# Performance work log

Measured on AMD Instinct MI355X. Metric: run time of the kernel, lower is better.

Reference implementation:

```python
import jax, jax.numpy as jnp
import numpy as np


def setup_inputs() -> dict:
    key = jax.random.key(0)
    ks = jax.random.split(key, 6)
    B, T, I, H, O = 64, 512, 256, 512, 256
    stdv = 1.0 / np.sqrt(H)
    u = lambda k, shape: jax.random.uniform(k, shape, jnp.float32, -stdv, stdv)
    return {
        "x": jax.random.normal(ks[0], (B, T, I), jnp.float32),
        "W": u(ks[1], (I, 4 * H)),
        "U": u(ks[2], (H, 4 * H)),
        "bias": u(ks[3], (4 * H,)),
        "Wl": u(ks[4], (H, O)),
        "bl": u(ks[5], (O,)),
    }


def lstm_scan(x, W, U, bias):
    B, T, I = x.shape
    H = U.shape[0]
    # Precompute input projections for all timesteps in one big GEMM: [B,T,4H]
    x_proj = jnp.einsum("bti,ig->btg", x, W) + bias

    def step(carry, xp_t):
        h, c = carry
        gates = xp_t + h @ U  # [B, 4H]
        i_t = jax.nn.sigmoid(gates[:, :H])
        f_t = jax.nn.sigmoid(gates[:, H:2 * H])
        g_t = jnp.tanh(gates[:, 2 * H:3 * H])
        o_t = jax.nn.sigmoid(gates[:, 3 * H:])
        c_new = f_t * c + i_t * g_t
        h_new = o_t * jnp.tanh(c_new)
        return (h_new, c_new), h_new

    h0 = jnp.zeros((B, H), x.dtype)
    c0 = jnp.zeros((B, H), x.dtype)
    (h_T, c_T), hs = jax.lax.scan(step, (h0, c0), jnp.swapaxes(x_proj, 0, 1))
    hidden_seq = jnp.swapaxes(hs, 0, 1)  # [B, T, H]
    return hidden_seq, h_T, c_T


def reference(x, W, U, bias, Wl, bl):
    hidden_seq, h_T, c_T = lstm_scan(x, W, U, bias)
    out = hidden_seq @ Wl + bl  # [B, T, O]
    return out, (h_T, c_T)
```

## Files before the change

### kernel.cpp

```cpp
#include <hip/hip_runtime.h>
#include <stdint.h>

typedef uint16_t u16;
typedef uint32_t u32;
typedef unsigned long long u64;
typedef __attribute__((ext_vector_type(8))) __bf16 bf16x8;
typedef __attribute__((ext_vector_type(8))) short short8;
typedef __attribute__((ext_vector_type(4))) float floatx4;

__device__ __forceinline__ float bf2f(u16 u) {
  union { u32 i; float f; } v; v.i = ((u32)u) << 16; return v.f;
}
__device__ __forceinline__ u16 f2bf(float f) {
  union { float f; u32 i; } v; v.f = f;
  u32 i = v.i;
  return (u16)((i + 0x7FFFu + ((i >> 16) & 1u)) >> 16);
}
__device__ __forceinline__ float sigm(float x) { return 1.f / (1.f + __expf(-x)); }
__device__ __forceinline__ float tanh_f(float x) {
  x = fminf(15.f, fmaxf(-15.f, x));
  float e = __expf(2.f * x);
  return (e - 1.f) / (e + 1.f);
}

__global__ void transpose_f32_bf16(const float* __restrict__ src, u16* __restrict__ dst,
                                   int R, int C) {
  __shared__ u16 tile[32][33];
  int x = blockIdx.x * 32 + threadIdx.x;
#pragma unroll
  for (int j = 0; j < 4; ++j) {
    int y = blockIdx.y * 32 + threadIdx.y + j * 8;
    if (x < C && y < R) tile[threadIdx.y + j * 8][threadIdx.x] = f2bf(src[(size_t)y * C + x]);
  }
  __syncthreads();
  int x2 = blockIdx.y * 32 + threadIdx.x;
#pragma unroll
  for (int j = 0; j < 4; ++j) {
    int y2 = blockIdx.x * 32 + threadIdx.y + j * 8;
    if (x2 < R && y2 < C) dst[(size_t)y2 * R + x2] = tile[threadIdx.x][threadIdx.y + j * 8];
  }
}

#define T_STEPS 512
#define HLSZ (16 * 520)
#define NWORK 224

#define LSTM_STEP(XC, XN, TT)                                                  \
  {                                                                            \
    const int t = (TT);                                                        \
    const int tn = (t + 1) & (T_STEPS - 1);                                    \
          \
    if (((tn) & 63) == 0 && t < T_STEPS - 1) {                                 \
      _Pragma("unroll")                                                        \
      for (int r = 0; r < 4; ++r) {                                            \
        const u32* cc = ctr + ((g * 16 + q4 * 4 + r) * 8 + (tn >> 6));         \
        while (__hip_atomic_load(cc, __ATOMIC_RELAXED,                         \
                                 __HIP_MEMORY_SCOPE_AGENT) < 32u)              \
          __builtin_amdgcn_s_sleep(2);                                         \
      }                                                                        \
      __asm__ volatile("" ::: "memory");                                       \
    }                                                                          \
                   \
    _Pragma("unroll")                                                          \
    for (int qg = 0; qg < 4; ++qg)                                             \
      _Pragma("unroll")                                                        \
      for (int r = 0; r < 4; ++r)                                              \
        XN[qg * 4 + r] = xp_base[((size_t)(q4 * 4 + r) * T_STEPS + tn) * 2048  \
                                 + qg * 512 + cb + n];                         \
    __asm__ volatile("" ::: "memory");                                         \
    floatx4 acc[4] = {};                                                       \
    if (t > 0) {                                                               \
      const u64* hsrc = (const u64*)(hT_all)                                   \
                        + (size_t)(g * T_STEPS + (t - 1)) * 2048;              \
      u64 v[8];                                                                \
      for (;;) {                                                               \
        _Pragma("unroll")                                                      \
        for (int it = 0; it < 8; ++it)                                         \
          v[it] = __hip_atomic_load(hsrc + it * 256 + tid, __ATOMIC_RELAXED,   \
                                    __HIP_MEMORY_SCOPE_AGENT);                 \
        bool ok = true;                                                        \
        _Pragma("unroll")                                                      \
        for (int it = 0; it < 8; ++it) ok &= (v[it] != ~0ull);                 \
        if (ok) break;                                                         \
      }                                                                        \
      __asm__ volatile("" ::: "memory");                                       \
      u16* buf = hls + ((t - 1) & 1) * HLSZ;                                   \
      _Pragma("unroll")                                                        \
      for (int it = 0; it < 8; ++it) {                                         \
        int idx = it * 256 + tid;                                              \
        int tile = idx >> 6, w = idx & 63;                                     \
        *(u64*)(buf + (w >> 2) * 520 + tile * 16 + (w & 3) * 4) = v[it];       \
      }                                                                        \
      __syncthreads();                                                         \
      _Pragma("unroll")                                                        \
      for (int kt = 0; kt < 16; ++kt) {                                        \
        bf16x8 a = *(const bf16x8*)(buf + n * 520 + kt * 32 + q4 * 8);         \
        acc[0] = __builtin_amdgcn_mfma_f32_16x16x32_bf16(a, u[0][kt], acc[0], 0, 0, 0); \
        acc[1] = __builtin_amdgcn_mfma_f32_16x16x32_bf16(a, u[1][kt], acc[1], 0, 0, 0); \
        acc[2] = __builtin_amdgcn_mfma_f32_16x16x32_bf16(a, u[2][kt], acc[2], 0, 0, 0); \
        acc[3] = __builtin_amdgcn_mfma_f32_16x16x32_bf16(a, u[3][kt], acc[3], 0, 0, 0); \
      }                                                                        \
    }                                                                          \
    _Pragma("unroll")                                                          \
    for (int r = 0; r < 4; ++r) {                                              \
      float gi = sigm(acc[0][r] + bf2f(XC[r]));                                \
      float gf = sigm(acc[1][r] + bf2f(XC[4 + r]));                            \
      float gg = tanh_f(acc[2][r] + bf2f(XC[8 + r]));                          \
      float go = sigm(acc[3][r] + bf2f(XC[12 + r]));                           \
      float cn = gf * cst[r] + gi * gg;                                        \
      cst[r] = cn;                                                             \
      float hv = go * tanh_f(cn);                                              \
      int row = q4 * 4 + r;                                                    \
      hp[row * 16 + n] = f2bf(hv);                                             \
      if (t == T_STEPS - 1) {                                                  \
        out_hT[(g * 16 + row) * 512 + cb + n] = hv;                            \
        out_cT[(g * 16 + row) * 512 + cb + n] = cn;                            \
      }                                                                        \
    }                                                                          \
    __asm__ volatile("s_waitcnt lgkmcnt(0)" ::: "memory");                     \
    {                                                                          \
      u64 v = *(const u64*)(hp + (lane >> 2) * 16 + (lane & 3) * 4);           \
      u64* hdst = (u64*)(hT_all) + (size_t)(g * T_STEPS + t) * 2048            \
                  + p * 64 + lane;                                             \
      __hip_atomic_store(hdst, v, __ATOMIC_RELAXED, __HIP_MEMORY_SCOPE_AGENT); \
    }                                                                          \
  }

__global__ __launch_bounds__(256, 1) void fused_lstm(
    const float* __restrict__ x,
    const u16* __restrict__ WT,
    const float* __restrict__ bias,
    u16* __restrict__ xp,
    const u16* __restrict__ UT,
    u16* __restrict__ hT_all,
    const u16* __restrict__ WlT,
    const float* __restrict__ bl,
    float* __restrict__ outC,
    float* __restrict__ out_hT,
    float* __restrict__ out_cT,
    u32* __restrict__ ctr) {
  __shared__ __align__(16) u16 smem[2 * HLSZ + 4 * 256];
  const int bi = blockIdx.x;
  const int tid = threadIdx.x;

  if (bi >= 32) {
    u16* As = smem;
    u16* Bs = smem + 64 * 40;
    const int wid = bi - 32;
    const int wave = tid >> 6, lane = tid & 63;
    const int q4 = lane >> 4, n16 = lane & 15;
    const int mw = (wave >> 1) * 32, nw = (wave & 1) * 32;
    const int ldrow = tid >> 2, ldseg = (tid & 3) * 8;

    for (int j = wid; j < 16384; j += NWORK) {
      const int tch = j >> 11;
      const int rem = j & 2047;
      const int b = rem >> 5, nt = rem & 31;
      const int m0 = b * 512 + tch * 64, n0 = nt * 64;
      floatx4 acc[2][2] = {};
      for (int k0 = 0; k0 < 256; k0 += 32) {
        const float* ap = x + (size_t)(m0 + ldrow) * 256 + k0 + ldseg;
        floatx4 a0 = *(const floatx4*)ap;
        floatx4 a1 = *(const floatx4*)(ap + 4);
        short8 s;
        s[0] = (short)f2bf(a0[0]); s[1] = (short)f2bf(a0[1]);
        s[2] = (short)f2bf(a0[2]); s[3] = (short)f2bf(a0[3]);
        s[4] = (short)f2bf(a1[0]); s[5] = (short)f2bf(a1[1]);
        s[6] = (short)f2bf(a1[2]); s[7] = (short)f2bf(a1[3]);
        *(short8*)(As + ldrow * 40 + ldseg) = s;
        *(short8*)(Bs + ldrow * 40 + ldseg) =
            *(const short8*)(WT + (size_t)(n0 + ldrow) * 256 + k0 + ldseg);
        __syncthreads();
#pragma unroll
        for (int mi = 0; mi < 2; ++mi) {
          bf16x8 a = *(const bf16x8*)(As + (mw + mi * 16 + n16) * 40 + q4 * 8);
#pragma unroll
          for (int ni = 0; ni < 2; ++ni) {
            bf16x8 bb = *(const bf16x8*)(Bs + (nw + ni * 16 + n16) * 40 + q4 * 8);
            acc[mi][ni] = __builtin_amdgcn_mfma_f32_16x16x32_bf16(a, bb, acc[mi][ni], 0, 0, 0);
          }
        }
        __syncthreads();
      }
#pragma unroll
      for (int mi = 0; mi < 2; ++mi)
#pragma unroll
        for (int ni = 0; ni < 2; ++ni) {
          int col = n0 + nw + ni * 16 + n16;
          float bv = bias[col];
#pragma unroll
          for (int r = 0; r < 4; ++r) {
            int m = m0 + mw + mi * 16 + q4 * 4 + r;
            u16 val = f2bf(acc[mi][ni][r] + bv);
            __hip_atomic_store(xp + (size_t)m * 2048 + col, val,
                               __ATOMIC_RELAXED, __HIP_MEMORY_SCOPE_AGENT);
          }
        }
      __asm__ volatile("s_waitcnt vmcnt(0)" ::: "memory");
      __syncthreads();
      if (tid == 0)
        __hip_atomic_fetch_add(ctr + b * 8 + tch, 1u,
                               __ATOMIC_RELAXED, __HIP_MEMORY_SCOPE_AGENT);
    }

    for (int j = wid; j < 2048; j += NWORK) {
      const int tb = j >> 4, g2 = (j >> 2) & 3, nt = j & 3;
      const int m0 = g2 * 8192 + tb * 64, n0 = nt * 64;
      const int mm = m0 + ldrow;
      const size_t slot = ((size_t)((mm >> 13) * 512 + ((mm & 8191) >> 4))) * 8192
                          + (mm & 15) * 16;
      floatx4 acc[2][2] = {};
      for (int k0 = 0; k0 < 512; k0 += 32) {
        int kk = k0 + ldseg;
        const u64* ap64 = (const u64*)(hT_all + slot + (kk >> 4) * 256 + (kk & 15));
        u64 lo, hi;
        for (;;) {
          lo = __hip_atomic_load(ap64, __ATOMIC_RELAXED, __HIP_MEMORY_SCOPE_AGENT);
          hi = __hip_atomic_load(ap64 + 1, __ATOMIC_RELAXED, __HIP_MEMORY_SCOPE_AGENT);
          if (lo != ~0ull && hi != ~0ull) break;
          __builtin_amdgcn_s_sleep(8);
        }
        *(u64*)(As + ldrow * 40 + ldseg) = lo;
        *(u64*)(As + ldrow * 40 + ldseg + 4) = hi;
        *(short8*)(Bs + ldrow * 40 + ldseg) =
            *(const short8*)(WlT + (size_t)(n0 + ldrow) * 512 + k0 + ldseg);
        __syncthreads();
#pragma unroll
        for (int mi = 0; mi < 2; ++mi) {
          bf16x8 a = *(const bf16x8*)(As + (mw + mi * 16 + n16) * 40 + q4 * 8);
#pragma unroll
          for (int ni = 0; ni < 2; ++ni) {
            bf16x8 bb = *(const bf16x8*)(Bs + (nw + ni * 16 + n16) * 40 + q4 * 8);
            acc[mi][ni] = __builtin_amdgcn_mfma_f32_16x16x32_bf16(a, bb, acc[mi][ni], 0, 0, 0);
          }
        }
        __syncthreads();
      }
#pragma unroll
      for (int mi = 0; mi < 2; ++mi)
#pragma unroll
        for (int ni = 0; ni < 2; ++ni) {
          int col = n0 + nw + ni * 16 + n16;
          float bv = bl[col];
#pragma unroll
          for (int r = 0; r < 4; ++r) {
            int m = m0 + mw + mi * 16 + q4 * 4 + r;
            int orow = ((m >> 13) * 16 + (m & 15)) * 512 + ((m & 8191) >> 4);
            outC[(size_t)orow * 256 + col] = acc[mi][ni][r] + bv;
          }
        }
    }
    return;
  }

  u16* hls = smem;
  u16* hstw = smem + 2 * HLSZ;
  const int g = (bi & 7) >> 1;
  const int wgi = ((bi & 1) << 2) | (bi >> 3);
  const int wave = tid >> 6;
  const int lane = tid & 63;
  const int n = lane & 15;
  const int q4 = lane >> 4;
  const int cb = wgi * 64 + wave * 16;
  const int p = wgi * 4 + wave;
  u16* hp = hstw + wave * 256;

  bf16x8 u[4][16];
#pragma unroll
  for (int qg = 0; qg < 4; ++qg) {
    const u16* up = UT + (size_t)(qg * 512 + cb + n) * 512;
#pragma unroll
    for (int kt = 0; kt < 16; ++kt)
      u[qg][kt] = *(const bf16x8*)(up + kt * 32 + q4 * 8);
  }

  float cst[4] = {0.f, 0.f, 0.f, 0.f};
  const u16* xp_base = xp + (size_t)(g * 16) * T_STEPS * 2048;

#pragma unroll
  for (int r = 0; r < 4; ++r) {
    const u32* cc = ctr + ((g * 16 + q4 * 4 + r) * 8 + 0);
    while (__hip_atomic_load(cc, __ATOMIC_RELAXED, __HIP_MEMORY_SCOPE_AGENT) < 32u)
      __builtin_amdgcn_s_sleep(2);
  }
  __asm__ volatile("" ::: "memory");

  u16 xa[16], xb[16];
#pragma unroll
  for (int qg = 0; qg < 4; ++qg)
#pragma unroll
    for (int r = 0; r < 4; ++r)
      xa[qg * 4 + r] = xp_base[((size_t)(q4 * 4 + r) * T_STEPS + 0) * 2048
                               + qg * 512 + cb + n];

#pragma unroll 1
  for (int t2 = 0; t2 < T_STEPS; t2 += 2) {
    LSTM_STEP(xa, xb, t2)
    LSTM_STEP(xb, xa, t2 + 1)
  }
}

extern "C" void kernel_launch(void* const* d_in, const int* in_sizes, int n_in,
                              void* d_out, int out_size, void* d_ws, size_t ws_size,
                              hipStream_t stream) {
  (void)in_sizes; (void)n_in; (void)out_size; (void)ws_size;
  const float* x    = (const float*)d_in[0];
  const float* W    = (const float*)d_in[1];
  const float* U    = (const float*)d_in[2];
  const float* bias = (const float*)d_in[3];
  const float* Wl   = (const float*)d_in[4];
  const float* bl   = (const float*)d_in[5];
  float* out = (float*)d_out;
  char* ws = (char*)d_ws;

  u16* xp     = (u16*)(ws + 0);
  u16* UT     = (u16*)(ws + 134217728);
  u16* WT     = (u16*)(ws + 136314880);
  u16* WlT    = (u16*)(ws + 137363456);
  u16* hT_all = (u16*)(ws + 137625600);

  u32* ctr = (u32*)(out + 8388608);

  hipMemsetAsync(hT_all, 0xFF, 33554432, stream);
  hipMemsetAsync(ctr, 0x00, 2048, stream);

  transpose_f32_bf16<<<dim3(2048 / 32, 256 / 32), dim3(32, 8), 0, stream>>>(W, WT, 256, 2048);
  transpose_f32_bf16<<<dim3(2048 / 32, 512 / 32), dim3(32, 8), 0, stream>>>(U, UT, 512, 2048);
  transpose_f32_bf16<<<dim3(256 / 32, 512 / 32), dim3(32, 8), 0, stream>>>(Wl, WlT, 512, 256);

  fused_lstm<<<256, 256, 0, stream>>>(x, WT, bias, xp, UT, hT_all, WlT, bl,
                                      out, out + 8388608, out + 8421376, ctr);
}
```

Measured before the change: 1.441 ms.

## Fuse weight transposes into persistent kernel and add per-step progress counters

```diff
diff --git a/kernel.cpp b/kernel.cpp
--- a/kernel.cpp
+++ b/kernel.cpp
@@ -23,24 +23,6 @@
   return (e - 1.f) / (e + 1.f);
 }
 
-__global__ void transpose_f32_bf16(const float* __restrict__ src, u16* __restrict__ dst,
-                                   int R, int C) {
-  __shared__ u16 tile[32][33];
-  int x = blockIdx.x * 32 + threadIdx.x;
-#pragma unroll
-  for (int j = 0; j < 4; ++j) {
-    int y = blockIdx.y * 32 + threadIdx.y + j * 8;
-    if (x < C && y < R) tile[threadIdx.y + j * 8][threadIdx.x] = f2bf(src[(size_t)y * C + x]);
-  }
-  __syncthreads();
-  int x2 = blockIdx.y * 32 + threadIdx.x;
-#pragma unroll
-  for (int j = 0; j < 4; ++j) {
-    int y2 = blockIdx.x * 32 + threadIdx.y + j * 8;
-    if (x2 < R && y2 < C) dst[(size_t)y2 * R + x2] = tile[threadIdx.x][threadIdx.y + j * 8];
-  }
-}
-
 #define T_STEPS 512
 #define HLSZ (16 * 520)
 #define NWORK 224
@@ -51,14 +33,15 @@
     const int tn = (t + 1) & (T_STEPS - 1);                                    \
           \
     if (((tn) & 63) == 0 && t < T_STEPS - 1) {                                 \
-      _Pragma("unroll")                                                        \
-      for (int r = 0; r < 4; ++r) {                                            \
-        const u32* cc = ctr + ((g * 16 + q4 * 4 + r) * 8 + (tn >> 6));         \
-        while (__hip_atomic_load(cc, __ATOMIC_RELAXED,                         \
-                                 __HIP_MEMORY_SCOPE_AGENT) < 32u)              \
-          __builtin_amdgcn_s_sleep(2);                                         \
-      }                                                                        \
-      __asm__ volatile("" ::: "memory");                                       \
+      if (tid == 0) {                                                          \
+        for (int rr = 0; rr < 16; ++rr) {                                      \
+          const u32* cc = xpctr + ((g * 16 + rr) * 8 + (tn >> 6));             \
+          while (__hip_atomic_load(cc, __ATOMIC_RELAXED,                       \
+                                   __HIP_MEMORY_SCOPE_AGENT) < 32u)            \
+            __builtin_amdgcn_s_sleep(2);                                       \
+        }                                                                      \
+      }                                                                        \
+      __syncthreads();                                                         \
     }                                                                          \
                    \
     _Pragma("unroll")                                                          \
@@ -124,17 +107,28 @@
                   + p * 64 + lane;                                             \
       __hip_atomic_store(hdst, v, __ATOMIC_RELAXED, __HIP_MEMORY_SCOPE_AGENT); \
     }                                                                          \
+              \
+    if ((t & 15) == 15) {                                                      \
+      __asm__ volatile("s_waitcnt vmcnt(0)" ::: "memory");                     \
+      __syncthreads();                                                         \
+      if (tid == 0)                                                            \
+        __hip_atomic_fetch_add(sctr + bi, 1u, __ATOMIC_RELAXED,                \
+                               __HIP_MEMORY_SCOPE_AGENT);                      \
+    }                                                                          \
   }
 
 __global__ __launch_bounds__(256, 1) void fused_lstm(
     const float* __restrict__ x,
-    const u16* __restrict__ WT,
+    const float* __restrict__ W,
+    const float* __restrict__ U,
     const float* __restrict__ bias,
+    const float* __restrict__ Wl,
+    const float* __restrict__ bl,
     u16* __restrict__ xp,
-    const u16* __restrict__ UT,
+    u16* __restrict__ WT,
+    u16* __restrict__ UT,
+    u16* __restrict__ WlT,
     u16* __restrict__ hT_all,
-    const u16* __restrict__ WlT,
-    const float* __restrict__ bl,
     float* __restrict__ outC,
     float* __restrict__ out_hT,
     float* __restrict__ out_cT,
@@ -142,15 +136,53 @@
   __shared__ __align__(16) u16 smem[2 * HLSZ + 4 * 256];
   const int bi = blockIdx.x;
   const int tid = threadIdx.x;
+  u32* xpctr = ctr;
+  u32* tctr = ctr + 512;
+  u32* sctr = ctr + 520;
 
   if (bi >= 32) {
-    u16* As = smem;
-    u16* Bs = smem + 64 * 40;
     const int wid = bi - 32;
     const int wave = tid >> 6, lane = tid & 63;
     const int q4 = lane >> 4, n16 = lane & 15;
     const int mw = (wave >> 1) * 32, nw = (wave & 1) * 32;
     const int ldrow = tid >> 2, ldseg = (tid & 3) * 8;
+    u16* As = smem;
+    u16* Bs = smem + 64 * 40;
+
+    {
+      u16* tlds = smem;
+      const int tx = tid & 31, ty = tid >> 5;
+      for (int j = wid; j < 1664; j += NWORK) {
+        const float* src; u16* dst; int R, C, bx, by, mat;
+        if (j < 1024)      { src = U;  dst = UT;  R = 512; C = 2048; bx = j & 63;          by = j >> 6;          mat = 0; }
+        else if (j < 1536) { src = W;  dst = WT;  R = 256; C = 2048; bx = (j - 1024) & 63; by = (j - 1024) >> 6; mat = 1; }
+        else               { src = Wl; dst = WlT; R = 512; C = 256;  bx = (j - 1536) & 7;  by = (j - 1536) >> 3; mat = 2; }
+        int xx = bx * 32 + tx;
+#pragma unroll
+        for (int jj = 0; jj < 4; ++jj) {
+          int yy = by * 32 + ty + jj * 8;
+          tlds[(ty + jj * 8) * 33 + tx] = f2bf(src[(size_t)yy * C + xx]);
+        }
+        __syncthreads();
+        int x2 = by * 32 + tx;
+#pragma unroll
+        for (int jj = 0; jj < 4; ++jj) {
+          int y2 = bx * 32 + ty + jj * 8;
+          __hip_atomic_store(dst + (size_t)y2 * R + x2, tlds[tx * 33 + ty + jj * 8],
+                             __ATOMIC_RELAXED, __HIP_MEMORY_SCOPE_AGENT);
+        }
+        __asm__ volatile("s_waitcnt vmcnt(0)" ::: "memory");
+        __syncthreads();
+        if (tid == 0)
+          __hip_atomic_fetch_add(tctr + mat, 1u, __ATOMIC_RELAXED,
+                                 __HIP_MEMORY_SCOPE_AGENT);
+      }
+    }
+    if (tid == 0)
+      while (__hip_atomic_load(tctr + 1, __ATOMIC_RELAXED,
+                               __HIP_MEMORY_SCOPE_AGENT) < 512u)
+        __builtin_amdgcn_s_sleep(2);
+    __syncthreads();
 
     for (int j = wid; j < 16384; j += NWORK) {
       const int tch = j >> 11;
@@ -199,9 +231,15 @@
       __asm__ volatile("s_waitcnt vmcnt(0)" ::: "memory");
       __syncthreads();
       if (tid == 0)
-        __hip_atomic_fetch_add(ctr + b * 8 + tch, 1u,
+        __hip_atomic_fetch_add(xpctr + b * 8 + tch, 1u,
                                __ATOMIC_RELAXED, __HIP_MEMORY_SCOPE_AGENT);
     }
+
+    if (tid == 0)
+      while (__hip_atomic_load(tctr + 2, __ATOMIC_RELAXED,
+                               __HIP_MEMORY_SCOPE_AGENT) < 128u)
+        __builtin_amdgcn_s_sleep(2);
+    __syncthreads();
 
     for (int j = wid; j < 2048; j += NWORK) {
       const int tb = j >> 4, g2 = (j >> 2) & 3, nt = j & 3;
@@ -209,6 +247,26 @@
       const int mm = m0 + ldrow;
       const size_t slot = ((size_t)((mm >> 13) * 512 + ((mm & 8191) >> 4))) * 8192
                           + (mm & 15) * 16;
+      const u32 need = (u32)(((tb * 4 + 3) >> 4) + 1);
+      if (tid == 0) {
+        int spins = 0;
+        for (;;) {
+          u32 mn = 0xFFFFFFFFu;
+#pragma unroll
+          for (int k = 0; k < 4; ++k)
+#pragma unroll
+            for (int e = 0; e < 2; ++e) {
+              u32 vv = __hip_atomic_load(sctr + ((k << 3) | (g2 * 2 + e)),
+                                         __ATOMIC_RELAXED, __HIP_MEMORY_SCOPE_AGENT);
+              mn = mn < vv ? mn : vv;
+            }
+          if (mn >= need) break;
+          if (++spins > 100000) break;
+          __builtin_amdgcn_s_sleep(16);
+        }
+      }
+      __syncthreads();
+
       floatx4 acc[2][2] = {};
       for (int k0 = 0; k0 < 512; k0 += 32) {
         int kk = k0 + ldseg;
@@ -265,6 +323,12 @@
   const int p = wgi * 4 + wave;
   u16* hp = hstw + wave * 256;
 
+  if (tid == 0)
+    while (__hip_atomic_load(tctr + 0, __ATOMIC_RELAXED,
+                             __HIP_MEMORY_SCOPE_AGENT) < 1024u)
+      __builtin_amdgcn_s_sleep(2);
+  __syncthreads();
+
   bf16x8 u[4][16];
 #pragma unroll
   for (int qg = 0; qg < 4; ++qg) {
@@ -277,13 +341,15 @@
   float cst[4] = {0.f, 0.f, 0.f, 0.f};
   const u16* xp_base = xp + (size_t)(g * 16) * T_STEPS * 2048;
 
-#pragma unroll
-  for (int r = 0; r < 4; ++r) {
-    const u32* cc = ctr + ((g * 16 + q4 * 4 + r) * 8 + 0);
-    while (__hip_atomic_load(cc, __ATOMIC_RELAXED, __HIP_MEMORY_SCOPE_AGENT) < 32u)
-      __builtin_amdgcn_s_sleep(2);
-  }
-  __asm__ volatile("" ::: "memory");
+  if (tid == 0) {
+    for (int rr = 0; rr < 16; ++rr) {
+      const u32* cc = xpctr + ((g * 16 + rr) * 8 + 0);
+      while (__hip_atomic_load(cc, __ATOMIC_RELAXED,
+                               __HIP_MEMORY_SCOPE_AGENT) < 32u)
+        __builtin_amdgcn_s_sleep(2);
+    }
+  }
+  __syncthreads();
 
   u16 xa[16], xb[16];
 #pragma unroll
@@ -322,12 +388,9 @@
   u32* ctr = (u32*)(out + 8388608);
 
   hipMemsetAsync(hT_all, 0xFF, 33554432, stream);
-  hipMemsetAsync(ctr, 0x00, 2048, stream);
-
-  transpose_f32_bf16<<<dim3(2048 / 32, 256 / 32), dim3(32, 8), 0, stream>>>(W, WT, 256, 2048);
-  transpose_f32_bf16<<<dim3(2048 / 32, 512 / 32), dim3(32, 8), 0, stream>>>(U, UT, 512, 2048);
-  transpose_f32_bf16<<<dim3(256 / 32, 512 / 32), dim3(32, 8), 0, stream>>>(Wl, WlT, 512, 256);
-
-  fused_lstm<<<256, 256, 0, stream>>>(x, WT, bias, xp, UT, hT_all, WlT, bl,
+  hipMemsetAsync(ctr, 0x00, 4096, stream);
+
+  fused_lstm<<<256, 256, 0, stream>>>(x, W, U, bias, Wl, bl,
+                                      xp, WT, UT, WlT, hT_all,
                                       out, out + 8388608, out + 8421376, ctr);
 }
```

After: 1.480 ms. 1.03x slower.
